# Kernel optimization log

Hardware: AMD Instinct MI355X
Metric: run time of the kernel (lower is better)

Reference implementation:

```python
import jax, jax.numpy as jnp
import numpy as np

NUM_HEADS = 6

def setup_inputs() -> dict:
    key = jax.random.key(0)
    ks = jax.random.split(key, 6)
    B_, N, C = 4096, 64, 192
    nW = 4096
    return {
        "x": jax.random.normal(ks[0], (B_, N, C), dtype=jnp.float32),
        "mask": jax.random.normal(ks[1], (nW, N, N), dtype=jnp.float32),
        "qkv_w": jax.random.normal(ks[2], (3 * C, C), dtype=jnp.float32) * 0.02,
        "qkv_b": jax.random.normal(ks[3], (3 * C,), dtype=jnp.float32) * 0.02,
        "proj_w": jax.random.normal(ks[4], (C, C), dtype=jnp.float32) * 0.02,
        "proj_b": jax.random.normal(ks[5], (C,), dtype=jnp.float32) * 0.02,
    }

def reference(x, mask, qkv_w, qkv_b, proj_w, proj_b):
    B_, N, C = x.shape
    H = NUM_HEADS
    hd = C // H
    scale = hd ** -0.5
    qkv = (x @ qkv_w.T + qkv_b).reshape(B_, N, 3, H, hd)
    qkv = jnp.transpose(qkv, (2, 0, 3, 1, 4))  # [3, B_, H, N, hd]
    q, k, v = qkv[0], qkv[1], qkv[2]
    attn = jnp.einsum('bhnd,bhmd->bhnm', q * scale, k)  # [B_, H, N, N]
    nW = mask.shape[0]
    # additive relative/shift mask broadcast over image batch and heads
    attn = attn.reshape(B_ // nW, nW, H, N, N) + mask[None, :, None, :, :]
    attn = attn.reshape(B_, H, N, N)
    attn = jax.nn.softmax(attn, axis=-1)
    out = jnp.einsum('bhnm,bhmd->bhnd', attn, v)  # [B_, H, N, hd]
    out = jnp.transpose(out, (0, 2, 1, 3)).reshape(B_, N, C)
    return out @ proj_w.T + proj_b
```

## Files before the change

kernel.cpp:

```cpp
#include <hip/hip_runtime.h>
#include <hip/hip_bf16.h>
#include <stdint.h>


#define NTOK 64
#define CDIM 192
#define KROW 40
#define VROW 72

typedef __attribute__((ext_vector_type(4))) float f32x4;
typedef __attribute__((ext_vector_type(8))) short bf16x8;

__device__ __forceinline__ short f2bf(float f) {
  __hip_bfloat16 h = __float2bfloat16(f);
  return *reinterpret_cast<short*>(&h);
}
__device__ __forceinline__ uint32_t pack2(float a, float b) {
  __hip_bfloat162 h2;
  h2.x = __float2bfloat16(a);
  h2.y = __float2bfloat16(b);
  return *reinterpret_cast<uint32_t*>(&h2);
}

__device__ __forceinline__ bf16x8 xpose(uint32_t A0, uint32_t A1,
                                        uint32_t B0, uint32_t B1,
                                        int s0, int s1, int hiSel) {
  uint32_t w[4];
  uint32_t a, b;
  a = (uint32_t)__shfl((int)A0, s0); b = (uint32_t)__shfl((int)B0, s0); w[0] = hiSel ? b : a;
  a = (uint32_t)__shfl((int)A1, s0); b = (uint32_t)__shfl((int)B1, s0); w[1] = hiSel ? b : a;
  a = (uint32_t)__shfl((int)A0, s1); b = (uint32_t)__shfl((int)B0, s1); w[2] = hiSel ? b : a;
  a = (uint32_t)__shfl((int)A1, s1); b = (uint32_t)__shfl((int)B1, s1); w[3] = hiSel ? b : a;
  return *reinterpret_cast<bf16x8*>(w);
}

#define GLOAD16(g, l) __builtin_amdgcn_global_load_lds( \
    (const __attribute__((address_space(1))) void*)(g), \
    (__attribute__((address_space(3))) void*)(l), 16, 0, 0)

__global__ void wconv_kernel(const float* __restrict__ qkv_w,
                             const float* __restrict__ proj_w,
                             short* __restrict__ ws) {
  const int r = blockIdx.x, c = threadIdx.x;
  int chunk, lr;
  float val;
  if (r < 192)      { chunk = r >> 5;                        lr = r & 31;         val = qkv_w[r * CDIM + c]; }
  else if (r < 384) { int q = r - 192; chunk = 6 + 2 * (q >> 5); lr = q & 31;     val = qkv_w[r * CDIM + c]; }
  else if (r < 576) { int q = r - 384; chunk = 7 + 2 * (q >> 5); lr = q & 31;     val = qkv_w[r * CDIM + c]; }
  else              { int q = r - 576; chunk = 18 + (q >> 5);    lr = q & 31;     val = proj_w[q * CDIM + c]; }
  const int s = c >> 3, lo = c & 7;
  const int sp = (s & 24) | ((s ^ lr) & 7);
  ws[chunk * 6144 + lr * CDIM + sp * 8 + lo] = f2bf(val);
}

__device__ __forceinline__ void stage32(short* __restrict__ dst,
                                        const short* __restrict__ src, int tid) {
  const int w = tid >> 6, lane = tid & 63;
  #pragma unroll
  for (int it = 0; it < 3; ++it) {
    const int cidx = it * 4 + w;
    GLOAD16(src + cidx * 512 + lane * 8, dst + cidx * 512);
  }
}

__global__ __launch_bounds__(256, 4)
void winattn_kernel(const float* __restrict__ x, const float* __restrict__ mask,
                    const short* __restrict__ ws,
                    const float* __restrict__ qkv_b, const float* __restrict__ proj_b,
                    float* __restrict__ out) {
  __shared__ __align__(16) short wbA[32 * CDIM];
  __shared__ __align__(16) short wbB[32 * CDIM];
  __shared__ __align__(16) short kh[NTOK * KROW];
  __shared__ __align__(16) short vth[2][32 * VROW];

  const int b    = blockIdx.x;
  const int tid  = threadIdx.x;
  const int lane = tid & 63;
  const int l16  = lane & 15;
  const int g4   = lane >> 4;
  const int m0   = (tid >> 6) * 16;
  const float scale = 0.17677669529663687f;
  const int s0 = (((2 * g4) & 3) << 4) + l16;
  const int s1 = (((2 * g4 + 1) & 3) << 4) + l16;
  const int hiSel = g4 >> 1;

  int soff[6];
  #pragma unroll
  for (int ks = 0; ks < 6; ++ks) {
    const int s = ks * 4 + g4;
    soff[ks] = ((s & 24) | ((s ^ l16) & 7)) << 3;
  }

  stage32(wbA, ws, tid);
  stage32(wbB, ws + 6144, tid);

  const float* xr = x + (size_t)b * (NTOK * CDIM) + (m0 + l16) * CDIM;
  bf16x8 af[6];
  #pragma unroll
  for (int ks = 0; ks < 6; ++ks) {
    const float4 v0 = *reinterpret_cast<const float4*>(xr + ks * 32 + g4 * 8);
    const float4 v1 = *reinterpret_cast<const float4*>(xr + ks * 32 + g4 * 8 + 4);
    uint32_t t[4];
    t[0] = pack2(v0.x, v0.y); t[1] = pack2(v0.z, v0.w);
    t[2] = pack2(v1.x, v1.y); t[3] = pack2(v1.z, v1.w);
    af[ks] = *reinterpret_cast<bf16x8*>(t);
  }
  const float* mrowl = mask + (size_t)b * (NTOK * NTOK) + (m0 + l16) * NTOK;

  __syncthreads();

  bf16x8 aq[6];
  #pragma unroll
  for (int c = 0; c < 6; ++c) {
    short* wb = (c & 1) ? wbB : wbA;
    uint32_t u[2][2];
    #pragma unroll
    for (int lct = 0; lct < 2; ++lct) {
      f32x4 acc = {0.f, 0.f, 0.f, 0.f};
      #pragma unroll
      for (int ks = 0; ks < 6; ++ks) {
        bf16x8 wf = *reinterpret_cast<const bf16x8*>(wb + (lct * 16 + l16) * CDIM + soff[ks]);
        acc = __builtin_amdgcn_mfma_f32_16x16x32_bf16(wf, af[ks], acc, 0, 0, 0);
      }
      const float4 bq = *reinterpret_cast<const float4*>(qkv_b + 32 * c + 16 * lct + 4 * g4);
      u[lct][0] = pack2((acc[0] + bq.x) * scale, (acc[1] + bq.y) * scale);
      u[lct][1] = pack2((acc[2] + bq.z) * scale, (acc[3] + bq.w) * scale);
    }
    aq[c] = xpose(u[0][0], u[0][1], u[1][0], u[1][1], s0, s1, hiSel);
    __syncthreads();
    stage32(wb, ws + (c + 2) * 6144, tid);
  }

  bf16x8 of[6];
  bf16x8 bpa, bpb;
  #pragma unroll
  for (int h = 0; h < 6; ++h) {
    #pragma unroll
    for (int lct = 0; lct < 2; ++lct) {
      f32x4 acc = {0.f, 0.f, 0.f, 0.f};
      #pragma unroll
      for (int ks = 0; ks < 6; ++ks) {
        bf16x8 wf = *reinterpret_cast<const bf16x8*>(wbA + (lct * 16 + l16) * CDIM + soff[ks]);
        acc = __builtin_amdgcn_mfma_f32_16x16x32_bf16(wf, af[ks], acc, 0, 0, 0);
      }
      const float4 bk4 = *reinterpret_cast<const float4*>(qkv_b + 192 + 32 * h + 16 * lct + 4 * g4);
      uint2 kw;
      kw.x = pack2(acc[0] + bk4.x, acc[1] + bk4.y);
      kw.y = pack2(acc[2] + bk4.z, acc[3] + bk4.w);
      *reinterpret_cast<uint2*>(kh + (m0 + l16) * KROW + 16 * lct + 4 * g4) = kw;
    }
    if (h > 0) {
      const int vp = (h - 1) & 1;
      uint32_t uo[2][2];
      #pragma unroll
      for (int ct2 = 0; ct2 < 2; ++ct2) {
        const short* vb = vth[vp] + (16 * ct2 + l16) * VROW;
        bf16x8 bv1 = *reinterpret_cast<const bf16x8*>(vb + g4 * 8);
        bf16x8 bv2 = *reinterpret_cast<const bf16x8*>(vb + 32 + g4 * 8);
        f32x4 acc = {0.f, 0.f, 0.f, 0.f};
        acc = __builtin_amdgcn_mfma_f32_16x16x32_bf16(bv1, bpa, acc, 0, 0, 0);
        acc = __builtin_amdgcn_mfma_f32_16x16x32_bf16(bv2, bpb, acc, 0, 0, 0);
        uo[ct2][0] = pack2(acc[0], acc[1]);
        uo[ct2][1] = pack2(acc[2], acc[3]);
      }
      of[h - 1] = xpose(uo[0][0], uo[0][1], uo[1][0], uo[1][1], s0, s1, hiSel);
    }
    __syncthreads();
    stage32(wbA, ws + (8 + 2 * h) * 6144, tid);

    #pragma unroll
    for (int lct = 0; lct < 2; ++lct) {
      f32x4 acc = {0.f, 0.f, 0.f, 0.f};
      #pragma unroll
      for (int ks = 0; ks < 6; ++ks) {
        bf16x8 wf = *reinterpret_cast<const bf16x8*>(wbB + (lct * 16 + l16) * CDIM + soff[ks]);
        acc = __builtin_amdgcn_mfma_f32_16x16x32_bf16(af[ks], wf, acc, 0, 0, 0);
      }
      const float bv = qkv_b[384 + 32 * h + 16 * lct + l16];
      uint2 vw;
      vw.x = pack2(acc[0] + bv, acc[1] + bv);
      vw.y = pack2(acc[2] + bv, acc[3] + bv);
      *reinterpret_cast<uint2*>(vth[h & 1] + (16 * lct + l16) * VROW + m0 + 4 * g4) = vw;
    }
    {
      float pr[4][4];
      float rmax = -1e30f;
      #pragma unroll
      for (int rt = 0; rt < 4; ++rt) {
        bf16x8 bk = *reinterpret_cast<const bf16x8*>(kh + (rt * 16 + l16) * KROW + g4 * 8);
        f32x4 z = {0.f, 0.f, 0.f, 0.f};
        f32x4 s = __builtin_amdgcn_mfma_f32_16x16x32_bf16(bk, aq[h], z, 0, 0, 0);
        const float4 mv = *reinterpret_cast<const float4*>(mrowl + 16 * rt + 4 * g4);
        pr[rt][0] = s[0] + mv.x; pr[rt][1] = s[1] + mv.y;
        pr[rt][2] = s[2] + mv.z; pr[rt][3] = s[3] + mv.w;
        #pragma unroll
        for (int i = 0; i < 4; ++i) rmax = fmaxf(rmax, pr[rt][i]);
      }
      rmax = fmaxf(rmax, __shfl_xor(rmax, 16));
      rmax = fmaxf(rmax, __shfl_xor(rmax, 32));
      float rsum = 0.f;
      #pragma unroll
      for (int rt = 0; rt < 4; ++rt)
        #pragma unroll
        for (int i = 0; i < 4; ++i) { pr[rt][i] = __expf(pr[rt][i] - rmax); rsum += pr[rt][i]; }
      rsum += __shfl_xor(rsum, 16);
      rsum += __shfl_xor(rsum, 32);
      const float rinv = 1.f / rsum;
      uint32_t wpk[4][2];
      #pragma unroll
      for (int rt = 0; rt < 4; ++rt) {
        wpk[rt][0] = pack2(pr[rt][0] * rinv, pr[rt][1] * rinv);
        wpk[rt][1] = pack2(pr[rt][2] * rinv, pr[rt][3] * rinv);
      }
      bpa = xpose(wpk[0][0], wpk[0][1], wpk[1][0], wpk[1][1], s0, s1, hiSel);
      bpb = xpose(wpk[2][0], wpk[2][1], wpk[3][0], wpk[3][1], s0, s1, hiSel);
    }
    __syncthreads();
    stage32(wbB, ws + (9 + 2 * h) * 6144, tid);
  }

  float* og = out + (size_t)b * (NTOK * CDIM);
  #pragma unroll
  for (int j = 0; j < 6; ++j) {
    const int c = 18 + j;
    short* wb = (c & 1) ? wbB : wbA;
    if (j == 0) {
      uint32_t uo[2][2];
      #pragma unroll
      for (int ct2 = 0; ct2 < 2; ++ct2) {
        const short* vb = vth[1] + (16 * ct2 + l16) * VROW;
        bf16x8 bv1 = *reinterpret_cast<const bf16x8*>(vb + g4 * 8);
        bf16x8 bv2 = *reinterpret_cast<const bf16x8*>(vb + 32 + g4 * 8);
        f32x4 acc = {0.f, 0.f, 0.f, 0.f};
        acc = __builtin_amdgcn_mfma_f32_16x16x32_bf16(bv1, bpa, acc, 0, 0, 0);
        acc = __builtin_amdgcn_mfma_f32_16x16x32_bf16(bv2, bpb, acc, 0, 0, 0);
        uo[ct2][0] = pack2(acc[0], acc[1]);
        uo[ct2][1] = pack2(acc[2], acc[3]);
      }
      of[5] = xpose(uo[0][0], uo[0][1], uo[1][0], uo[1][1], s0, s1, hiSel);
    }
    #pragma unroll
    for (int lct = 0; lct < 2; ++lct) {
      f32x4 acc = {0.f, 0.f, 0.f, 0.f};
      #pragma unroll
      for (int ks = 0; ks < 6; ++ks) {
        bf16x8 wf = *reinterpret_cast<const bf16x8*>(wb + (lct * 16 + l16) * CDIM + soff[ks]);
        acc = __builtin_amdgcn_mfma_f32_16x16x32_bf16(of[ks], wf, acc, 0, 0, 0);
      }
      const int cc = 32 * j + 16 * lct + l16;
      const float pb = proj_b[cc];
      #pragma unroll
      for (int i = 0; i < 4; ++i)
        og[(m0 + 4 * g4 + i) * CDIM + cc] = acc[i] + pb;
    }
    if (j < 5) {
      __syncthreads();
      if (j < 4) stage32(wb, ws + (c + 2) * 6144, tid);
    }
  }
}

extern "C" void kernel_launch(void* const* d_in, const int* in_sizes, int n_in,
                              void* d_out, int out_size, void* d_ws, size_t ws_size,
                              hipStream_t stream) {
  const float* x      = (const float*)d_in[0];
  const float* mask   = (const float*)d_in[1];
  const float* qkv_w  = (const float*)d_in[2];
  const float* qkv_b  = (const float*)d_in[3];
  const float* proj_w = (const float*)d_in[4];
  const float* proj_b = (const float*)d_in[5];
  float* out = (float*)d_out;

  short* ws = (short*)d_ws;

  wconv_kernel<<<768, 192, 0, stream>>>(qkv_w, proj_w, ws);
  winattn_kernel<<<4096, 256, 0, stream>>>(x, mask, ws, qkv_b, proj_b, out);
}
```

Baseline: 231.1 us.

## Halve weight staging chunks to 16 rows and raise occupancy to 6 blocks

Weight chunks staged into LDS shrink from 32 to 16 output rows, so the double buffers take half the shared memory. The V transpose buffer is no longer double-buffered, and launch bounds are raised from 4 to 6 blocks per CU. All projection loops are restructured to walk twice as many half-size chunks, which roughly doubles the number of __syncthreads barriers and staging rounds. The aim is to hide global and LDS latency through higher occupancy, at the cost of more synchronisation and tighter register limits.

```diff
diff --git a/kernel.cpp b/kernel.cpp
--- a/kernel.cpp
+++ b/kernel.cpp
@@ -7,6 +7,7 @@
 #define CDIM 192
 #define KROW 40
 #define VROW 72
+#define CHUNK 3072
 
 typedef __attribute__((ext_vector_type(4))) float f32x4;
 typedef __attribute__((ext_vector_type(8))) short bf16x8;
@@ -44,34 +45,33 @@
   const int r = blockIdx.x, c = threadIdx.x;
   int chunk, lr;
   float val;
-  if (r < 192)      { chunk = r >> 5;                        lr = r & 31;         val = qkv_w[r * CDIM + c]; }
-  else if (r < 384) { int q = r - 192; chunk = 6 + 2 * (q >> 5); lr = q & 31;     val = qkv_w[r * CDIM + c]; }
-  else if (r < 576) { int q = r - 384; chunk = 7 + 2 * (q >> 5); lr = q & 31;     val = qkv_w[r * CDIM + c]; }
-  else              { int q = r - 576; chunk = 18 + (q >> 5);    lr = q & 31;     val = proj_w[q * CDIM + c]; }
+  if (r < 192)      { chunk = r >> 4; lr = r & 15; val = qkv_w[r * CDIM + c]; }
+  else if (r < 384) { int q = r - 192; int h = q >> 5; int rr = q & 31;
+                      chunk = 12 + 4 * h + (rr >> 4); lr = rr & 15; val = qkv_w[r * CDIM + c]; }
+  else if (r < 576) { int q = r - 384; int h = q >> 5; int rr = q & 31;
+                      chunk = 14 + 4 * h + (rr >> 4); lr = rr & 15; val = qkv_w[r * CDIM + c]; }
+  else              { int q = r - 576; chunk = 36 + (q >> 4); lr = q & 15; val = proj_w[q * CDIM + c]; }
   const int s = c >> 3, lo = c & 7;
   const int sp = (s & 24) | ((s ^ lr) & 7);
-  ws[chunk * 6144 + lr * CDIM + sp * 8 + lo] = f2bf(val);
-}
-
-__device__ __forceinline__ void stage32(short* __restrict__ dst,
+  ws[chunk * CHUNK + lr * CDIM + sp * 8 + lo] = f2bf(val);
+}
+
+__device__ __forceinline__ void stage16(short* __restrict__ dst,
                                         const short* __restrict__ src, int tid) {
   const int w = tid >> 6, lane = tid & 63;
-  #pragma unroll
-  for (int it = 0; it < 3; ++it) {
-    const int cidx = it * 4 + w;
-    GLOAD16(src + cidx * 512 + lane * 8, dst + cidx * 512);
-  }
-}
-
-__global__ __launch_bounds__(256, 4)
+  GLOAD16(src + w * 512 + lane * 8, dst + w * 512);
+  if (w < 2) GLOAD16(src + (4 + w) * 512 + lane * 8, dst + (4 + w) * 512);
+}
+
+__global__ __launch_bounds__(256, 6)
 void winattn_kernel(const float* __restrict__ x, const float* __restrict__ mask,
                     const short* __restrict__ ws,
                     const float* __restrict__ qkv_b, const float* __restrict__ proj_b,
                     float* __restrict__ out) {
-  __shared__ __align__(16) short wbA[32 * CDIM];
-  __shared__ __align__(16) short wbB[32 * CDIM];
+  __shared__ __align__(16) short wbA[16 * CDIM];
+  __shared__ __align__(16) short wbB[16 * CDIM];
   __shared__ __align__(16) short kh[NTOK * KROW];
-  __shared__ __align__(16) short vth[2][32 * VROW];
+  __shared__ __align__(16) short vth[32 * VROW];
 
   const int b    = blockIdx.x;
   const int tid  = threadIdx.x;
@@ -91,8 +91,8 @@
     soff[ks] = ((s & 24) | ((s ^ l16) & 7)) << 3;
   }
 
-  stage32(wbA, ws, tid);
-  stage32(wbB, ws + 6144, tid);
+  stage16(wbA, ws, tid);
+  stage16(wbB, ws + CHUNK, tid);
 
   const float* xr = x + (size_t)b * (NTOK * CDIM) + (m0 + l16) * CDIM;
   bf16x8 af[6];
@@ -110,51 +110,48 @@
   __syncthreads();
 
   bf16x8 aq[6];
-  #pragma unroll
-  for (int c = 0; c < 6; ++c) {
+  uint32_t ue0 = 0, ue1 = 0;
+  #pragma unroll
+  for (int c = 0; c < 12; ++c) {
     short* wb = (c & 1) ? wbB : wbA;
-    uint32_t u[2][2];
+    f32x4 acc = {0.f, 0.f, 0.f, 0.f};
     #pragma unroll
-    for (int lct = 0; lct < 2; ++lct) {
-      f32x4 acc = {0.f, 0.f, 0.f, 0.f};
-      #pragma unroll
-      for (int ks = 0; ks < 6; ++ks) {
-        bf16x8 wf = *reinterpret_cast<const bf16x8*>(wb + (lct * 16 + l16) * CDIM + soff[ks]);
-        acc = __builtin_amdgcn_mfma_f32_16x16x32_bf16(wf, af[ks], acc, 0, 0, 0);
-      }
-      const float4 bq = *reinterpret_cast<const float4*>(qkv_b + 32 * c + 16 * lct + 4 * g4);
-      u[lct][0] = pack2((acc[0] + bq.x) * scale, (acc[1] + bq.y) * scale);
-      u[lct][1] = pack2((acc[2] + bq.z) * scale, (acc[3] + bq.w) * scale);
-    }
-    aq[c] = xpose(u[0][0], u[0][1], u[1][0], u[1][1], s0, s1, hiSel);
-    __syncthreads();
-    stage32(wb, ws + (c + 2) * 6144, tid);
+    for (int ks = 0; ks < 6; ++ks) {
+      bf16x8 wf = *reinterpret_cast<const bf16x8*>(wb + l16 * CDIM + soff[ks]);
+      acc = __builtin_amdgcn_mfma_f32_16x16x32_bf16(wf, af[ks], acc, 0, 0, 0);
+    }
+    const float4 bq = *reinterpret_cast<const float4*>(qkv_b + 16 * c + 4 * g4);
+    const uint32_t u0 = pack2((acc[0] + bq.x) * scale, (acc[1] + bq.y) * scale);
+    const uint32_t u1 = pack2((acc[2] + bq.z) * scale, (acc[3] + bq.w) * scale);
+    if (c & 1) aq[c >> 1] = xpose(ue0, ue1, u0, u1, s0, s1, hiSel);
+    else       { ue0 = u0; ue1 = u1; }
+    __syncthreads();
+    stage16(wb, ws + (c + 2) * CHUNK, tid);
   }
 
   bf16x8 of[6];
   bf16x8 bpa, bpb;
   #pragma unroll
   for (int h = 0; h < 6; ++h) {
-    #pragma unroll
-    for (int lct = 0; lct < 2; ++lct) {
+    const int base = 12 + 4 * h;
+    {
       f32x4 acc = {0.f, 0.f, 0.f, 0.f};
       #pragma unroll
       for (int ks = 0; ks < 6; ++ks) {
-        bf16x8 wf = *reinterpret_cast<const bf16x8*>(wbA + (lct * 16 + l16) * CDIM + soff[ks]);
+        bf16x8 wf = *reinterpret_cast<const bf16x8*>(wbA + l16 * CDIM + soff[ks]);
         acc = __builtin_amdgcn_mfma_f32_16x16x32_bf16(wf, af[ks], acc, 0, 0, 0);
       }
-      const float4 bk4 = *reinterpret_cast<const float4*>(qkv_b + 192 + 32 * h + 16 * lct + 4 * g4);
+      const float4 bk4 = *reinterpret_cast<const float4*>(qkv_b + 192 + 32 * h + 4 * g4);
       uint2 kw;
       kw.x = pack2(acc[0] + bk4.x, acc[1] + bk4.y);
       kw.y = pack2(acc[2] + bk4.z, acc[3] + bk4.w);
-      *reinterpret_cast<uint2*>(kh + (m0 + l16) * KROW + 16 * lct + 4 * g4) = kw;
+      *reinterpret_cast<uint2*>(kh + (m0 + l16) * KROW + 4 * g4) = kw;
     }
     if (h > 0) {
-      const int vp = (h - 1) & 1;
       uint32_t uo[2][2];
       #pragma unroll
       for (int ct2 = 0; ct2 < 2; ++ct2) {
-        const short* vb = vth[vp] + (16 * ct2 + l16) * VROW;
+        const short* vb = vth + (16 * ct2 + l16) * VROW;
         bf16x8 bv1 = *reinterpret_cast<const bf16x8*>(vb + g4 * 8);
         bf16x8 bv2 = *reinterpret_cast<const bf16x8*>(vb + 32 + g4 * 8);
         f32x4 acc = {0.f, 0.f, 0.f, 0.f};
@@ -166,21 +163,36 @@
       of[h - 1] = xpose(uo[0][0], uo[0][1], uo[1][0], uo[1][1], s0, s1, hiSel);
     }
     __syncthreads();
-    stage32(wbA, ws + (8 + 2 * h) * 6144, tid);
-
-    #pragma unroll
-    for (int lct = 0; lct < 2; ++lct) {
+    stage16(wbA, ws + (base + 2) * CHUNK, tid);
+
+    {
       f32x4 acc = {0.f, 0.f, 0.f, 0.f};
       #pragma unroll
       for (int ks = 0; ks < 6; ++ks) {
-        bf16x8 wf = *reinterpret_cast<const bf16x8*>(wbB + (lct * 16 + l16) * CDIM + soff[ks]);
+        bf16x8 wf = *reinterpret_cast<const bf16x8*>(wbB + l16 * CDIM + soff[ks]);
+        acc = __builtin_amdgcn_mfma_f32_16x16x32_bf16(wf, af[ks], acc, 0, 0, 0);
+      }
+      const float4 bk4 = *reinterpret_cast<const float4*>(qkv_b + 192 + 32 * h + 16 + 4 * g4);
+      uint2 kw;
+      kw.x = pack2(acc[0] + bk4.x, acc[1] + bk4.y);
+      kw.y = pack2(acc[2] + bk4.z, acc[3] + bk4.w);
+      *reinterpret_cast<uint2*>(kh + (m0 + l16) * KROW + 16 + 4 * g4) = kw;
+    }
+    __syncthreads();
+    stage16(wbB, ws + (base + 3) * CHUNK, tid);
+
+    {
+      f32x4 acc = {0.f, 0.f, 0.f, 0.f};
+      #pragma unroll
+      for (int ks = 0; ks < 6; ++ks) {
+        bf16x8 wf = *reinterpret_cast<const bf16x8*>(wbA + l16 * CDIM + soff[ks]);
         acc = __builtin_amdgcn_mfma_f32_16x16x32_bf16(af[ks], wf, acc, 0, 0, 0);
       }
-      const float bv = qkv_b[384 + 32 * h + 16 * lct + l16];
+      const float bv = qkv_b[384 + 32 * h + l16];
       uint2 vw;
       vw.x = pack2(acc[0] + bv, acc[1] + bv);
       vw.y = pack2(acc[2] + bv, acc[3] + bv);
-      *reinterpret_cast<uint2*>(vth[h & 1] + (16 * lct + l16) * VROW + m0 + 4 * g4) = vw;
+      *reinterpret_cast<uint2*>(vth + l16 * VROW + m0 + 4 * g4) = vw;
     }
     {
       float pr[4][4];
@@ -216,19 +228,34 @@
       bpb = xpose(wpk[2][0], wpk[2][1], wpk[3][0], wpk[3][1], s0, s1, hiSel);
     }
     __syncthreads();
-    stage32(wbB, ws + (9 + 2 * h) * 6144, tid);
+    stage16(wbA, ws + (h < 5 ? base + 4 : 36) * CHUNK, tid);
+
+    {
+      f32x4 acc = {0.f, 0.f, 0.f, 0.f};
+      #pragma unroll
+      for (int ks = 0; ks < 6; ++ks) {
+        bf16x8 wf = *reinterpret_cast<const bf16x8*>(wbB + l16 * CDIM + soff[ks]);
+        acc = __builtin_amdgcn_mfma_f32_16x16x32_bf16(af[ks], wf, acc, 0, 0, 0);
+      }
+      const float bv = qkv_b[384 + 32 * h + 16 + l16];
+      uint2 vw;
+      vw.x = pack2(acc[0] + bv, acc[1] + bv);
+      vw.y = pack2(acc[2] + bv, acc[3] + bv);
+      *reinterpret_cast<uint2*>(vth + (16 + l16) * VROW + m0 + 4 * g4) = vw;
+    }
+    __syncthreads();
+    stage16(wbB, ws + (h < 5 ? base + 5 : 37) * CHUNK, tid);
   }
 
   float* og = out + (size_t)b * (NTOK * CDIM);
   #pragma unroll
-  for (int j = 0; j < 6; ++j) {
-    const int c = 18 + j;
-    short* wb = (c & 1) ? wbB : wbA;
+  for (int j = 0; j < 12; ++j) {
+    short* wb = (j & 1) ? wbB : wbA;
     if (j == 0) {
       uint32_t uo[2][2];
       #pragma unroll
       for (int ct2 = 0; ct2 < 2; ++ct2) {
-        const short* vb = vth[1] + (16 * ct2 + l16) * VROW;
+        const short* vb = vth + (16 * ct2 + l16) * VROW;
         bf16x8 bv1 = *reinterpret_cast<const bf16x8*>(vb + g4 * 8);
         bf16x8 bv2 = *reinterpret_cast<const bf16x8*>(vb + 32 + g4 * 8);
         f32x4 acc = {0.f, 0.f, 0.f, 0.f};
@@ -239,23 +266,22 @@
       }
       of[5] = xpose(uo[0][0], uo[0][1], uo[1][0], uo[1][1], s0, s1, hiSel);
     }
+    f32x4 acc = {0.f, 0.f, 0.f, 0.f};
     #pragma unroll
-    for (int lct = 0; lct < 2; ++lct) {
-      f32x4 acc = {0.f, 0.f, 0.f, 0.f};
-      #pragma unroll
-      for (int ks = 0; ks < 6; ++ks) {
-        bf16x8 wf = *reinterpret_cast<const bf16x8*>(wb + (lct * 16 + l16) * CDIM + soff[ks]);
-        acc = __builtin_amdgcn_mfma_f32_16x16x32_bf16(of[ks], wf, acc, 0, 0, 0);
-      }
-      const int cc = 32 * j + 16 * lct + l16;
-      const float pb = proj_b[cc];
-      #pragma unroll
-      for (int i = 0; i < 4; ++i)
-        og[(m0 + 4 * g4 + i) * CDIM + cc] = acc[i] + pb;
-    }
-    if (j < 5) {
+    for (int ks = 0; ks < 6; ++ks) {
+      bf16x8 wf = *reinterpret_cast<const bf16x8*>(wb + l16 * CDIM + soff[ks]);
+      acc = __builtin_amdgcn_mfma_f32_16x16x32_bf16(of[ks], wf, acc, 0, 0, 0);
+    }
+    const int cc = 16 * j + l16;
+    const float pb = proj_b[cc];
+    #pragma unroll
+    for (int i = 0; i < 4; ++i)
+      og[(m0 + 4 * g4 + i) * CDIM + cc] = acc[i] + pb;
+    if (j < 10) {
       __syncthreads();
-      if (j < 4) stage32(wb, ws + (c + 2) * 6144, tid);
+      stage16(wb, ws + (38 + j) * CHUNK, tid);
+    } else if (j == 10) {
+      __syncthreads();
     }
   }
 }
```

New measurement: 402.9 us. 1.74x slower.
